# Optimization experiments

Measured on AMD Instinct MI355X. Metric: run time of the kernel, lower is better.

## Reference

```python
import jax, jax.numpy as jnp
from jax import lax
import numpy as np

BLANK = 0
PAD = 1
LABEL_SMOOTHING = 0.1
CE_SCALE = 1.0
TEMPERATURE = 1.0

B, T, U1, D, V = 8, 128, 33, 512, 4096  # U1 = U + 1


def setup_inputs() -> dict:
    key = jax.random.key(0)
    k0, k1, k2, k3, k4 = jax.random.split(key, 5)
    x = jax.random.normal(k0, (B, T, U1, D), dtype=jnp.float32)
    weight = jax.random.normal(k1, (V, D), dtype=jnp.float32) * 0.02
    bias = jnp.zeros((V,), dtype=jnp.float32)
    src_lengths = jax.random.randint(k2, (B,), T // 2, T + 1, dtype=jnp.int32)
    tgt_lengths = jax.random.randint(k3, (B,), U1 // 2, U1, dtype=jnp.int32)
    targets = jax.random.randint(k4, (B, U1 - 1), 2, V, dtype=jnp.int32)
    pos = jnp.arange(U1 - 1, dtype=jnp.int32)
    targets = jnp.where(pos[None, :] < tgt_lengths[:, None], targets, PAD)
    return {'x': x, 'weight': weight, 'bias': bias, 'targets': targets,
            'src_lengths': src_lengths, 'tgt_lengths': tgt_lengths}


def _rnnt_neglogp(blank_lp, emit_lp, src_lengths, tgt_lengths):
    """RNN-T forward DP. blank_lp: (B,T,U1) log P(blank); emit_lp: (B,T,U) log P(y_u).
    Returns per-utterance negative log-likelihood, shape (B,)."""
    Bn, Tn, U1n = blank_lp.shape
    # alpha at t=0: can only emit labels -> prefix-sum of emit log-probs
    alpha0 = jnp.concatenate(
        [jnp.zeros((Bn, 1), blank_lp.dtype), jnp.cumsum(emit_lp[:, 0, :], axis=1)], axis=1)

    def t_step(alpha_prev, xs):
        blank_prev, emit_t = xs  # (B,U1), (B,U)
        a = alpha_prev + blank_prev  # blank transition from t-1
        def u_step(c, xu):
            a_u, e_prev = xu  # each (B,)
            c = jnp.logaddexp(a_u, c + e_prev)  # emit transition from u-1 at same t
            return c, c
        _, rest = lax.scan(u_step, a[:, 0], (a[:, 1:].T, emit_t.T))  # rest: (U,B)
        alpha_t = jnp.concatenate([a[:, :1], rest.T], axis=1)
        return alpha_t, alpha_t

    xs = (jnp.swapaxes(blank_lp[:, :-1], 0, 1), jnp.swapaxes(emit_lp[:, 1:], 0, 1))
    _, alphas_rest = lax.scan(t_step, alpha0, xs)  # (T-1,B,U1)
    alphas = jnp.concatenate([alpha0[None], alphas_rest], axis=0)  # (T,B,U1)
    bidx = jnp.arange(Bn)
    alpha_last_t = alphas[src_lengths - 1, bidx]  # (B,U1)
    a_fin = jnp.take_along_axis(alpha_last_t, tgt_lengths[:, None], axis=1)[:, 0]
    b_fin = blank_lp[bidx, src_lengths - 1, tgt_lengths]  # final blank emission
    return -(a_fin + b_fin)


def reference(x, weight, bias, targets, src_lengths, tgt_lengths):
    Vn = weight.shape[0]
    # joint logits over full lattice: (B,T,U1,V)
    logits = (jnp.einsum('btud,vd->btuv', x, weight) + bias).astype(jnp.float32)
    lp = jax.nn.log_softmax(logits / TEMPERATURE, axis=-1)
    blank_lp = lp[..., BLANK]  # (B,T,U1)
    emit_lp = jnp.take_along_axis(lp[:, :, :-1, :], targets[:, None, :, None].astype(jnp.int32), axis=3)[..., 0]  # (B,T,U)
    loss_prob = jnp.sum(_rnnt_neglogp(blank_lp, emit_lp, src_lengths, tgt_lengths))
    loss_delay = jnp.zeros((), jnp.float32)  # delay_func == 'zero'
    # label-smoothed CE on last valid encoder frame
    last_h = jnp.take_along_axis(x, (src_lengths - 1)[:, None, None, None], axis=1)[:, 0]  # (B,U1,D)
    last_h = last_h[:, :-1]  # (B,U,D)
    ce_logits = (jnp.einsum('bud,vd->buv', last_h, weight) + bias).astype(jnp.float32)
    lprobs = jax.nn.log_softmax(ce_logits, axis=-1)
    nll = -jnp.take_along_axis(lprobs, targets[..., None], axis=-1)[..., 0]  # (B,U)
    smooth = -jnp.sum(lprobs, axis=-1)
    mask = (targets != PAD).astype(lprobs.dtype)
    eps_i = LABEL_SMOOTHING / (Vn - 1)
    loss_smoothed = jnp.sum(((1.0 - LABEL_SMOOTHING - eps_i) * nll + eps_i * smooth) * mask)
    total = loss_prob + loss_delay + CE_SCALE * loss_smoothed
    return total
```

## Files before the change

### kernel.cpp

```cpp
#include <hip/hip_runtime.h>
#include <hip/hip_bf16.h>
#include <math.h>
#include <stdint.h>

#define B_ 8
#define T_ 128
#define U1_ 33
#define D_ 512
#define V_ 4096
#define M_ (B_*T_*U1_)

#define BLANK_ 0
#define PAD_ 1

#define TM 128
#define TN 128
#define BKB 128
#define NK (D_/BKB)
#define GN (V_/TN)

typedef __attribute__((ext_vector_type(4))) float fvec4;
typedef __attribute__((ext_vector_type(8))) int   i8v;
typedef __attribute__((ext_vector_type(4))) int   i4v;

#define SCALE_A 0x7F7F7F7Fu
#define SCALE_B 0x79797979u

__device__ __forceinline__ void load_lds16(const uint8_t* g, uint8_t* l) {
    __builtin_amdgcn_global_load_lds(
        (const __attribute__((address_space(1))) unsigned int*)g,
        (__attribute__((address_space(3))) unsigned int*)l, 16, 0, 0);
}

__device__ __forceinline__ unsigned pack4_fp8(fvec4 v) {
    int r = __builtin_amdgcn_cvt_pk_fp8_f32(v.x, v.y, 0, false);
    r = __builtin_amdgcn_cvt_pk_fp8_f32(v.z, v.w, r, true);
    return (unsigned)r;
}

__global__ void convert_kernel(const float* __restrict__ x, const float* __restrict__ w,
                               uint8_t* __restrict__ xf8, uint8_t* __restrict__ wf8)
{
    int i = blockIdx.x * 256 + threadIdx.x;
    int stride = gridDim.x * 256;
    const int nx = (M_ * D_) / 16;
    const int nw = (V_ * D_) / 16;
    for (int j = i; j < nx; j += stride) {
        const fvec4* p = (const fvec4*)x + (size_t)j * 4;
        uint4 o = { pack4_fp8(p[0]), pack4_fp8(p[1]), pack4_fp8(p[2]), pack4_fp8(p[3]) };
        ((uint4*)xf8)[j] = o;
    }
    for (int j = i; j < nw; j += stride) {
        const fvec4* p = (const fvec4*)w + (size_t)j * 4;
        fvec4 v0 = p[0]*64.0f, v1 = p[1]*64.0f, v2 = p[2]*64.0f, v3 = p[3]*64.0f;
        uint4 o = { pack4_fp8(v0), pack4_fp8(v1), pack4_fp8(v2), pack4_fp8(v3) };
        ((uint4*)wf8)[j] = o;
    }
}

__global__ __launch_bounds__(256, 2)
void gemm_fused(const uint8_t* __restrict__ xf8, const uint8_t* __restrict__ wf8,
                const float* __restrict__ bias, const int* __restrict__ targets,
                float* __restrict__ partial_e, float* __restrict__ partial_z,
                float* __restrict__ blank_z, float* __restrict__ emit_z)
{
    __shared__ __align__(16) uint8_t As[2][TM * BKB];
    __shared__ __align__(16) uint8_t Bs[2][TN * BKB];
    __shared__ float ps[TM], pz[TM];
    __shared__ int tgt_s[TM];

    const int tid  = threadIdx.x;
    const int lane = tid & 63;
    const int wid  = tid >> 6;
    const int m0   = blockIdx.x * TM;
    const int n0   = blockIdx.y * TN;

    const int srow = wid * 32 + (lane >> 3);
    const int schk = (lane & 7) ^ ((lane >> 3) & 7);
    const uint8_t* agp = xf8 + (size_t)(m0 + srow) * D_ + schk * 16;
    const uint8_t* bgp = wf8 + (size_t)(n0 + srow) * D_ + schk * 16;

    fvec4 acc[4][4];
#pragma unroll
    for (int i = 0; i < 4; i++)
#pragma unroll
        for (int j = 0; j < 4; j++) acc[i][j] = (fvec4)0.0f;

    const int wrow = (wid >> 1) * 64;
    const int wcol = (wid & 1) * 64;
    const int m15  = lane & 15;
    const int quad = lane >> 4;

    auto stage = [&](int buf, int ks) {
        const uint8_t* ag = agp + ks * BKB;
        const uint8_t* bg = bgp + ks * BKB;
#pragma unroll
        for (int j = 0; j < 4; j++) {
            load_lds16(ag + j * 8 * D_, &As[buf][(wid * 32 + j * 8) * BKB]);
            load_lds16(bg + j * 8 * D_, &Bs[buf][(wid * 32 + j * 8) * BKB]);
        }
    };

    stage(0, 0);
    __syncthreads();

    const int e   = m15 & 7;
    const int c0b = (((quad << 1) ^ e) << 4);

    for (int ks = 0; ks < NK; ks++) {
        const int cur = ks & 1;
        if (ks + 1 < NK) stage(cur ^ 1, ks + 1);

        i8v fa[4], fb[4];
#pragma unroll
        for (int mi = 0; mi < 4; mi++) {
            int base = (wrow + mi * 16 + m15) << 7;
            union { i4v h[2]; i8v w; } u;
            u.h[0] = *(const i4v*)&As[cur][base + c0b];
            u.h[1] = *(const i4v*)&As[cur][base + (c0b ^ 16)];
            fa[mi] = u.w;
        }
#pragma unroll
        for (int ni = 0; ni < 4; ni++) {
            int base = (wcol + ni * 16 + m15) << 7;
            union { i4v h[2]; i8v w; } u;
            u.h[0] = *(const i4v*)&Bs[cur][base + c0b];
            u.h[1] = *(const i4v*)&Bs[cur][base + (c0b ^ 16)];
            fb[ni] = u.w;
        }
#pragma unroll
        for (int mi = 0; mi < 4; mi++)
#pragma unroll
            for (int ni = 0; ni < 4; ni++)
                acc[mi][ni] = __builtin_amdgcn_mfma_scale_f32_16x16x128_f8f6f4(
                                  fa[mi], fb[ni], acc[mi][ni],
                                  0, 0,
                                  0, SCALE_A, 0, SCALE_B);
        __syncthreads();
    }

    if (tid < TM) {
        ps[tid] = 0.0f; pz[tid] = 0.0f;
        int row = m0 + tid;
        int u = row % U1_;
        int b = row / (T_ * U1_);
        tgt_s[tid] = (u < U1_ - 1) ? targets[b * (U1_ - 1) + u] : -1;
    }
    __syncthreads();

    float bv[4];
#pragma unroll
    for (int ni = 0; ni < 4; ni++) bv[ni] = bias[n0 + wcol + ni * 16 + m15];

    const bool blank_lane = (blockIdx.y == 0) && (wcol == 0) && (m15 == 0);

#pragma unroll
    for (int mi = 0; mi < 4; mi++) {
#pragma unroll
        for (int r = 0; r < 4; r++) {
            const int irow = wrow + mi * 16 + quad * 4 + r;
            float se = 0.0f, sz = 0.0f;
#pragma unroll
            for (int ni = 0; ni < 4; ni++) {
                float z = acc[mi][ni][r] + bv[ni];
                se += __expf(z);
                sz += z;
                int c = n0 + wcol + ni * 16 + m15;
                if (tgt_s[irow] == c) emit_z[m0 + irow] = z;
            }
            if (blank_lane) blank_z[m0 + irow] = acc[mi][0][r] + bv[0];
            se += __shfl_xor(se, 1, 64); sz += __shfl_xor(sz, 1, 64);
            se += __shfl_xor(se, 2, 64); sz += __shfl_xor(sz, 2, 64);
            se += __shfl_xor(se, 4, 64); sz += __shfl_xor(sz, 4, 64);
            se += __shfl_xor(se, 8, 64); sz += __shfl_xor(sz, 8, 64);
            if (m15 == 0) { atomicAdd(&ps[irow], se); atomicAdd(&pz[irow], sz); }
        }
    }
    __syncthreads();
    if (tid < TM) {
        partial_e[(size_t)blockIdx.y * M_ + m0 + tid] = ps[tid];
        partial_z[(size_t)blockIdx.y * M_ + m0 + tid] = pz[tid];
    }
}

__global__ void lse_combine(const float* __restrict__ partial_e, const float* __restrict__ partial_z,
                            const float* __restrict__ emit_z, const int* __restrict__ targets,
                            const int* __restrict__ src_lengths,
                            float* __restrict__ lse, float* __restrict__ out)
{
    int r = blockIdx.x * 256 + threadIdx.x;
    float se = 0.0f, sz = 0.0f;
#pragma unroll
    for (int j = 0; j < GN; j++) {
        se += partial_e[(size_t)j * M_ + r];
        sz += partial_z[(size_t)j * M_ + r];
    }
    float l = __logf(se);
    lse[r] = l;

    int b   = r / (T_ * U1_);
    int rem = r % (T_ * U1_);
    int t   = rem / U1_;
    int u   = rem % U1_;
    if (u < U1_ - 1 && t == src_lengths[b] - 1) {
        int tgt = targets[b * (U1_ - 1) + u];
        if (tgt != PAD_) {
            float nll    = l - emit_z[r];
            float smooth = (float)V_ * l - sz;
            const float eps_i = 0.1f / (float)(V_ - 1);
            atomicAdd(out, (1.0f - 0.1f - eps_i) * nll + eps_i * smooth);
        }
    }
}

__global__ __launch_bounds__(256)
void dp_kernel(const float* __restrict__ blank_z, const float* __restrict__ emit_z,
               const float* __restrict__ lse, const int* __restrict__ src_lengths,
               const int* __restrict__ tgt_lengths, float* __restrict__ out)
{
    __shared__ float blp[T_ * U1_];
    __shared__ float elp[T_ * U1_];
    const int tid = threadIdx.x;
    const int b = blockIdx.x;
    for (int i = tid; i < T_ * U1_; i += 256) {
        int g = b * T_ * U1_ + i;
        float l = lse[g];
        blp[i] = blank_z[g] - l;
        elp[i] = emit_z[g] - l;
    }
    __syncthreads();
    if (tid >= 64) return;

    const int u = tid;
    const int ua = (u < U1_) ? u : U1_ - 1;
    const int sl = src_lengths[b], tl = tgt_lengths[b];

    float val = 0.0f;
    float afin = 0.0f;

    for (int d = 1; d <= (T_ - 1) + (U1_ - 1); d++) {
        int t = d - u;
        int tb = t - 1; tb = tb < 0 ? 0 : (tb > T_ - 1 ? T_ - 1 : tb);
        int tc = t < 0 ? 0 : (t > T_ - 1 ? T_ - 1 : t);
        float blv = blp[tb * U1_ + ua];
        float elv = elp[tc * U1_ + (ua > 0 ? ua - 1 : 0)];
        float up = __shfl_up(val, 1, 64);
        bool valid = (u < U1_) && (t >= 0) && (t < T_);
        if (valid) {
            if (t == 0) {
                val = up + elv;
            } else if (u == 0) {
                val = val + blv;
            } else {
                float a1 = val + blv;
                float a2 = up + elv;
                float mx = fmaxf(a1, a2), mn = fminf(a1, a2);
                val = mx + log1pf(__expf(mn - mx));
            }
            if (t == sl - 1 && u == tl) afin = val;
        }
    }
#pragma unroll
    for (int off = 1; off < 64; off <<= 1) afin += __shfl_xor(afin, off, 64);
    if (u == 0) {
        float bfin = blp[(sl - 1) * U1_ + tl];
        atomicAdd(out, -(afin + bfin));
    }
}

extern "C" void kernel_launch(void* const* d_in, const int* in_sizes, int n_in,
                              void* d_out, int out_size, void* d_ws, size_t ws_size,
                              hipStream_t stream)
{
    const float* x           = (const float*)d_in[0];
    const float* w           = (const float*)d_in[1];
    const float* bias        = (const float*)d_in[2];
    const int*   targets     = (const int*)d_in[3];
    const int*   src_lengths = (const int*)d_in[4];
    const int*   tgt_lengths = (const int*)d_in[5];
    float* out = (float*)d_out;

    char* p = (char*)d_ws;
    uint8_t* xf8 = (uint8_t*)p;     p += (size_t)M_ * D_;
    uint8_t* wf8 = (uint8_t*)p;     p += (size_t)V_ * D_;
    float* partial_e = (float*)p;   p += (size_t)GN * M_ * sizeof(float);
    float* partial_z = (float*)p;   p += (size_t)GN * M_ * sizeof(float);
    float* lse       = (float*)p;   p += (size_t)M_ * sizeof(float);
    float* blank_z   = (float*)p;   p += (size_t)M_ * sizeof(float);
    float* emit_z    = (float*)p;   p += (size_t)M_ * sizeof(float);

    hipMemsetAsync(out, 0, sizeof(float), stream);

    convert_kernel<<<1536, 256, 0, stream>>>(x, w, xf8, wf8);
    gemm_fused<<<dim3(M_/TM, V_/TN), 256, 0, stream>>>(xf8, wf8, bias, targets,
                                                       partial_e, partial_z, blank_z, emit_z);
    lse_combine<<<M_/256, 256, 0, stream>>>(partial_e, partial_z, emit_z, targets,
                                            src_lengths, lse, out);
    dp_kernel<<<B_, 256, 0, stream>>>(blank_z, emit_z, lse, src_lengths, tgt_lengths, out);
}
```

Baseline: 364.7 us.

## Keep A tile resident in LDS and loop over N tiles per block

After: 600.5 us. 1.65x slower.

```diff
diff --git a/kernel.cpp b/kernel.cpp
--- a/kernel.cpp
+++ b/kernel.cpp
@@ -14,10 +14,11 @@
 #define PAD_ 1
 
 #define TM 128
-#define TN 128
+#define TNS 256
 #define BKB 128
-#define NK (D_/BKB)
-#define GN (V_/TN)
+#define NKS (D_/BKB)
+#define GY 4
+#define NTILES (V_/(GY*TNS))
 
 typedef __attribute__((ext_vector_type(4))) float fvec4;
 typedef __attribute__((ext_vector_type(8))) int   i8v;
@@ -58,14 +59,14 @@
     }
 }
 
-__global__ __launch_bounds__(256, 2)
+__global__ __launch_bounds__(512, 2)
 void gemm_fused(const uint8_t* __restrict__ xf8, const uint8_t* __restrict__ wf8,
                 const float* __restrict__ bias, const int* __restrict__ targets,
                 float* __restrict__ partial_e, float* __restrict__ partial_z,
                 float* __restrict__ blank_z, float* __restrict__ emit_z)
 {
-    __shared__ __align__(16) uint8_t As[2][TM * BKB];
-    __shared__ __align__(16) uint8_t Bs[2][TN * BKB];
+    __shared__ __align__(16) uint8_t As[NKS][TM * BKB];
+    __shared__ __align__(16) uint8_t Bs[2][TNS * BKB];
     __shared__ float ps[TM], pz[TM];
     __shared__ int tgt_s[TM];
 
@@ -73,71 +74,25 @@
     const int lane = tid & 63;
     const int wid  = tid >> 6;
     const int m0   = blockIdx.x * TM;
-    const int n0   = blockIdx.y * TN;
-
-    const int srow = wid * 32 + (lane >> 3);
+    const int nslice = blockIdx.y;
+
     const int schk = (lane & 7) ^ ((lane >> 3) & 7);
-    const uint8_t* agp = xf8 + (size_t)(m0 + srow) * D_ + schk * 16;
-    const uint8_t* bgp = wf8 + (size_t)(n0 + srow) * D_ + schk * 16;
-
-    fvec4 acc[4][4];
-#pragma unroll
-    for (int i = 0; i < 4; i++)
-#pragma unroll
-        for (int j = 0; j < 4; j++) acc[i][j] = (fvec4)0.0f;
-
-    const int wrow = (wid >> 1) * 64;
-    const int wcol = (wid & 1) * 64;
-    const int m15  = lane & 15;
-    const int quad = lane >> 4;
-
-    auto stage = [&](int buf, int ks) {
-        const uint8_t* ag = agp + ks * BKB;
-        const uint8_t* bg = bgp + ks * BKB;
-#pragma unroll
-        for (int j = 0; j < 4; j++) {
-            load_lds16(ag + j * 8 * D_, &As[buf][(wid * 32 + j * 8) * BKB]);
+
+    auto stageB = [&](int buf, int nt, int ks) {
+        const uint8_t* bg = wf8 + (size_t)(nslice * (GY==4?1024:V_/GY) + nt * TNS
+                                           + wid * 32 + (lane >> 3)) * D_
+                                + ks * BKB + schk * 16;
+#pragma unroll
+        for (int j = 0; j < 4; j++)
             load_lds16(bg + j * 8 * D_, &Bs[buf][(wid * 32 + j * 8) * BKB]);
-        }
     };
-
-    stage(0, 0);
-    __syncthreads();
-
-    const int e   = m15 & 7;
-    const int c0b = (((quad << 1) ^ e) << 4);
-
-    for (int ks = 0; ks < NK; ks++) {
-        const int cur = ks & 1;
-        if (ks + 1 < NK) stage(cur ^ 1, ks + 1);
-
-        i8v fa[4], fb[4];
-#pragma unroll
-        for (int mi = 0; mi < 4; mi++) {
-            int base = (wrow + mi * 16 + m15) << 7;
-            union { i4v h[2]; i8v w; } u;
-            u.h[0] = *(const i4v*)&As[cur][base + c0b];
-            u.h[1] = *(const i4v*)&As[cur][base + (c0b ^ 16)];
-            fa[mi] = u.w;
-        }
-#pragma unroll
-        for (int ni = 0; ni < 4; ni++) {
-            int base = (wcol + ni * 16 + m15) << 7;
-            union { i4v h[2]; i8v w; } u;
-            u.h[0] = *(const i4v*)&Bs[cur][base + c0b];
-            u.h[1] = *(const i4v*)&Bs[cur][base + (c0b ^ 16)];
-            fb[ni] = u.w;
-        }
-#pragma unroll
-        for (int mi = 0; mi < 4; mi++)
-#pragma unroll
-            for (int ni = 0; ni < 4; ni++)
-                acc[mi][ni] = __builtin_amdgcn_mfma_scale_f32_16x16x128_f8f6f4(
-                                  fa[mi], fb[ni], acc[mi][ni],
-                                  0, 0,
-                                  0, SCALE_A, 0, SCALE_B);
-        __syncthreads();
-    }
+    auto stageA = [&](int ks) {
+        const uint8_t* ag = xf8 + (size_t)(m0 + wid * 16 + (lane >> 3)) * D_
+                                + ks * BKB + schk * 16;
+#pragma unroll
+        for (int j = 0; j < 2; j++)
+            load_lds16(ag + j * 8 * D_, &As[ks][(wid * 16 + j * 8) * BKB]);
+    };
 
     if (tid < TM) {
         ps[tid] = 0.0f; pz[tid] = 0.0f;
@@ -146,40 +101,95 @@
         int b = row / (T_ * U1_);
         tgt_s[tid] = (u < U1_ - 1) ? targets[b * (U1_ - 1) + u] : -1;
     }
+#pragma unroll
+    for (int ks = 0; ks < NKS; ks++) stageA(ks);
+    stageB(0, 0, 0);
     __syncthreads();
 
-    float bv[4];
-#pragma unroll
-    for (int ni = 0; ni < 4; ni++) bv[ni] = bias[n0 + wcol + ni * 16 + m15];
-
-    const bool blank_lane = (blockIdx.y == 0) && (wcol == 0) && (m15 == 0);
-
-#pragma unroll
-    for (int mi = 0; mi < 4; mi++) {
-#pragma unroll
-        for (int r = 0; r < 4; r++) {
-            const int irow = wrow + mi * 16 + quad * 4 + r;
-            float se = 0.0f, sz = 0.0f;
+    const int wrow = (wid >> 2) * 64;
+    const int wcol = (wid & 3) * 64;
+    const int m15  = lane & 15;
+    const int quad = lane >> 4;
+    const int e    = m15 & 7;
+    const int c0b  = (((quad << 1) ^ e) << 4);
+
+    int cur = 0;
+    for (int nt = 0; nt < NTILES; nt++) {
+        fvec4 acc[4][4];
+#pragma unroll
+        for (int i = 0; i < 4; i++)
+#pragma unroll
+            for (int j = 0; j < 4; j++) acc[i][j] = (fvec4)0.0f;
+
+#pragma unroll
+        for (int ks = 0; ks < NKS; ks++) {
+            if (ks < NKS - 1)           stageB(cur ^ 1, nt, ks + 1);
+            else if (nt < NTILES - 1)   stageB(cur ^ 1, nt + 1, 0);
+
+            i8v fa[4], fb[4];
+#pragma unroll
+            for (int mi = 0; mi < 4; mi++) {
+                int base = (wrow + mi * 16 + m15) << 7;
+                union { i4v h[2]; i8v w; } u;
+                u.h[0] = *(const i4v*)&As[ks][base + c0b];
+                u.h[1] = *(const i4v*)&As[ks][base + (c0b ^ 16)];
+                fa[mi] = u.w;
+            }
 #pragma unroll
             for (int ni = 0; ni < 4; ni++) {
-                float z = acc[mi][ni][r] + bv[ni];
-                se += __expf(z);
-                sz += z;
-                int c = n0 + wcol + ni * 16 + m15;
-                if (tgt_s[irow] == c) emit_z[m0 + irow] = z;
+                int base = (wcol + ni * 16 + m15) << 7;
+                union { i4v h[2]; i8v w; } u;
+                u.h[0] = *(const i4v*)&Bs[cur][base + c0b];
+                u.h[1] = *(const i4v*)&Bs[cur][base + (c0b ^ 16)];
+                fb[ni] = u.w;
             }
-            if (blank_lane) blank_z[m0 + irow] = acc[mi][0][r] + bv[0];
-            se += __shfl_xor(se, 1, 64); sz += __shfl_xor(sz, 1, 64);
-            se += __shfl_xor(se, 2, 64); sz += __shfl_xor(sz, 2, 64);
-            se += __shfl_xor(se, 4, 64); sz += __shfl_xor(sz, 4, 64);
-            se += __shfl_xor(se, 8, 64); sz += __shfl_xor(sz, 8, 64);
-            if (m15 == 0) { atomicAdd(&ps[irow], se); atomicAdd(&pz[irow], sz); }
+#pragma unroll
+            for (int mi = 0; mi < 4; mi++)
+#pragma unroll
+                for (int ni = 0; ni < 4; ni++)
+                    acc[mi][ni] = __builtin_amdgcn_mfma_scale_f32_16x16x128_f8f6f4(
+                                      fa[mi], fb[ni], acc[mi][ni],
+                                      0, 0,
+                                      0, SCALE_A, 0, SCALE_B);
+            __syncthreads();
+            cur ^= 1;
         }
-    }
+
+        const int nbase = nslice * (V_ / GY) + nt * TNS;
+        float bv[4];
+#pragma unroll
+        for (int ni = 0; ni < 4; ni++) bv[ni] = bias[nbase + wcol + ni * 16 + m15];
+
+        const bool blank_lane = (nslice == 0) && (nt == 0) && (wcol == 0) && (m15 == 0);
+
+#pragma unroll
+        for (int mi = 0; mi < 4; mi++) {
+#pragma unroll
+            for (int r = 0; r < 4; r++) {
+                const int irow = wrow + mi * 16 + quad * 4 + r;
+                float se = 0.0f, sz = 0.0f;
+#pragma unroll
+                for (int ni = 0; ni < 4; ni++) {
+                    float z = acc[mi][ni][r] + bv[ni];
+                    se += __expf(z);
+                    sz += z;
+                    int c = nbase + wcol + ni * 16 + m15;
+                    if (tgt_s[irow] == c) emit_z[m0 + irow] = z;
+                }
+                if (blank_lane) blank_z[m0 + irow] = acc[mi][0][r] + bv[0];
+                se += __shfl_xor(se, 1, 64); sz += __shfl_xor(sz, 1, 64);
+                se += __shfl_xor(se, 2, 64); sz += __shfl_xor(sz, 2, 64);
+                se += __shfl_xor(se, 4, 64); sz += __shfl_xor(sz, 4, 64);
+                se += __shfl_xor(se, 8, 64); sz += __shfl_xor(sz, 8, 64);
+                if (m15 == 0) { atomicAdd(&ps[irow], se); atomicAdd(&pz[irow], sz); }
+            }
+        }
+    }
+
     __syncthreads();
     if (tid < TM) {
-        partial_e[(size_t)blockIdx.y * M_ + m0 + tid] = ps[tid];
-        partial_z[(size_t)blockIdx.y * M_ + m0 + tid] = pz[tid];
+        partial_e[(size_t)nslice * M_ + m0 + tid] = ps[tid];
+        partial_z[(size_t)nslice * M_ + m0 + tid] = pz[tid];
     }
 }
 
@@ -191,7 +201,7 @@
     int r = blockIdx.x * 256 + threadIdx.x;
     float se = 0.0f, sz = 0.0f;
 #pragma unroll
-    for (int j = 0; j < GN; j++) {
+    for (int j = 0; j < GY; j++) {
         se += partial_e[(size_t)j * M_ + r];
         sz += partial_z[(size_t)j * M_ + r];
     }
@@ -283,8 +293,8 @@
     char* p = (char*)d_ws;
     uint8_t* xf8 = (uint8_t*)p;     p += (size_t)M_ * D_;
     uint8_t* wf8 = (uint8_t*)p;     p += (size_t)V_ * D_;
-    float* partial_e = (float*)p;   p += (size_t)GN * M_ * sizeof(float);
-    float* partial_z = (float*)p;   p += (size_t)GN * M_ * sizeof(float);
+    float* partial_e = (float*)p;   p += (size_t)GY * M_ * sizeof(float);
+    float* partial_z = (float*)p;   p += (size_t)GY * M_ * sizeof(float);
     float* lse       = (float*)p;   p += (size_t)M_ * sizeof(float);
     float* blank_z   = (float*)p;   p += (size_t)M_ * sizeof(float);
     float* emit_z    = (float*)p;   p += (size_t)M_ * sizeof(float);
@@ -292,8 +302,8 @@
     hipMemsetAsync(out, 0, sizeof(float), stream);
 
     convert_kernel<<<1536, 256, 0, stream>>>(x, w, xf8, wf8);
-    gemm_fused<<<dim3(M_/TM, V_/TN), 256, 0, stream>>>(xf8, wf8, bias, targets,
-                                                       partial_e, partial_z, blank_z, emit_z);
+    gemm_fused<<<dim3(M_/TM, GY), 512, 0, stream>>>(xf8, wf8, bias, targets,
+                                                    partial_e, partial_z, blank_z, emit_z);
     lse_combine<<<M_/256, 256, 0, stream>>>(partial_e, partial_z, emit_z, targets,
                                             src_lengths, lse, out);
     dp_kernel<<<B_, 256, 0, stream>>>(blank_z, emit_z, lse, src_lengths, tgt_lengths, out);
```

## Compute smoothing logit sum via column-summed weights and tighten GEMM pipeline barriers

Applied to the files above, without the earlier changes.

Result: slower. 452.4 us (+24.0%).

```diff
diff --git a/kernel.cpp b/kernel.cpp
--- a/kernel.cpp
+++ b/kernel.cpp
@@ -58,15 +58,34 @@
     }
 }
 
+__global__ void wsum_kernel(const float* __restrict__ w, const float* __restrict__ bias,
+                            float* __restrict__ wsum)
+{
+    const int t = threadIdx.x;
+    const int v0 = blockIdx.x * 128;
+    float s0 = 0.0f, s1 = 0.0f;
+    for (int v = 0; v < 128; v++) {
+        s0 += w[(size_t)(v0 + v) * D_ + t];
+        s1 += w[(size_t)(v0 + v) * D_ + t + 256];
+    }
+    atomicAdd(&wsum[t], s0);
+    atomicAdd(&wsum[t + 256], s1);
+    if (blockIdx.x == 0) {
+        float b = 0.0f;
+        for (int v = t; v < V_; v += 256) b += bias[v];
+        atomicAdd(&wsum[D_], b);
+    }
+}
+
 __global__ __launch_bounds__(256, 2)
 void gemm_fused(const uint8_t* __restrict__ xf8, const uint8_t* __restrict__ wf8,
                 const float* __restrict__ bias, const int* __restrict__ targets,
-                float* __restrict__ partial_e, float* __restrict__ partial_z,
+                float* __restrict__ partial_e,
                 float* __restrict__ blank_z, float* __restrict__ emit_z)
 {
     __shared__ __align__(16) uint8_t As[2][TM * BKB];
     __shared__ __align__(16) uint8_t Bs[2][TN * BKB];
-    __shared__ float ps[TM], pz[TM];
+    __shared__ float ps[TM];
     __shared__ int tgt_s[TM];
 
     const int tid  = threadIdx.x;
@@ -102,6 +121,13 @@
     };
 
     stage(0, 0);
+    if (tid < TM) {
+        ps[tid] = 0.0f;
+        int row = m0 + tid;
+        int u = row % U1_;
+        int b = row / (T_ * U1_);
+        tgt_s[tid] = (u < U1_ - 1) ? targets[b * (U1_ - 1) + u] : -1;
+    }
     __syncthreads();
 
     const int e   = m15 & 7;
@@ -109,7 +135,14 @@
 
     for (int ks = 0; ks < NK; ks++) {
         const int cur = ks & 1;
-        if (ks + 1 < NK) stage(cur ^ 1, ks + 1);
+        if (ks + 1 < NK) {
+            stage(cur ^ 1, ks + 1);
+            asm volatile("s_waitcnt vmcnt(8)" ::: "memory");
+        } else {
+            asm volatile("s_waitcnt vmcnt(0)" ::: "memory");
+        }
+        __builtin_amdgcn_sched_barrier(0);
+        __builtin_amdgcn_s_barrier();
 
         i8v fa[4], fb[4];
 #pragma unroll
@@ -136,17 +169,9 @@
                                   fa[mi], fb[ni], acc[mi][ni],
                                   0, 0,
                                   0, SCALE_A, 0, SCALE_B);
-        __syncthreads();
-    }
-
-    if (tid < TM) {
-        ps[tid] = 0.0f; pz[tid] = 0.0f;
-        int row = m0 + tid;
-        int u = row % U1_;
-        int b = row / (T_ * U1_);
-        tgt_s[tid] = (u < U1_ - 1) ? targets[b * (U1_ - 1) + u] : -1;
-    }
-    __syncthreads();
+        __builtin_amdgcn_s_barrier();
+        __builtin_amdgcn_sched_barrier(0);
+    }
 
     float bv[4];
 #pragma unroll
@@ -159,42 +184,38 @@
 #pragma unroll
         for (int r = 0; r < 4; r++) {
             const int irow = wrow + mi * 16 + quad * 4 + r;
-            float se = 0.0f, sz = 0.0f;
+            float se = 0.0f;
 #pragma unroll
             for (int ni = 0; ni < 4; ni++) {
                 float z = acc[mi][ni][r] + bv[ni];
                 se += __expf(z);
-                sz += z;
                 int c = n0 + wcol + ni * 16 + m15;
                 if (tgt_s[irow] == c) emit_z[m0 + irow] = z;
             }
             if (blank_lane) blank_z[m0 + irow] = acc[mi][0][r] + bv[0];
-            se += __shfl_xor(se, 1, 64); sz += __shfl_xor(sz, 1, 64);
-            se += __shfl_xor(se, 2, 64); sz += __shfl_xor(sz, 2, 64);
-            se += __shfl_xor(se, 4, 64); sz += __shfl_xor(sz, 4, 64);
-            se += __shfl_xor(se, 8, 64); sz += __shfl_xor(sz, 8, 64);
-            if (m15 == 0) { atomicAdd(&ps[irow], se); atomicAdd(&pz[irow], sz); }
+            se += __shfl_xor(se, 1, 64);
+            se += __shfl_xor(se, 2, 64);
+            se += __shfl_xor(se, 4, 64);
+            se += __shfl_xor(se, 8, 64);
+            if (m15 == 0) atomicAdd(&ps[irow], se);
         }
     }
     __syncthreads();
     if (tid < TM) {
         partial_e[(size_t)blockIdx.y * M_ + m0 + tid] = ps[tid];
-        partial_z[(size_t)blockIdx.y * M_ + m0 + tid] = pz[tid];
-    }
-}
-
-__global__ void lse_combine(const float* __restrict__ partial_e, const float* __restrict__ partial_z,
+    }
+}
+
+__global__ void lse_combine(const float* __restrict__ partial_e,
                             const float* __restrict__ emit_z, const int* __restrict__ targets,
                             const int* __restrict__ src_lengths,
+                            const float* __restrict__ x, const float* __restrict__ wsum,
                             float* __restrict__ lse, float* __restrict__ out)
 {
     int r = blockIdx.x * 256 + threadIdx.x;
-    float se = 0.0f, sz = 0.0f;
-#pragma unroll
-    for (int j = 0; j < GN; j++) {
-        se += partial_e[(size_t)j * M_ + r];
-        sz += partial_z[(size_t)j * M_ + r];
-    }
+    float se = 0.0f;
+#pragma unroll
+    for (int j = 0; j < GN; j++) se += partial_e[(size_t)j * M_ + r];
     float l = __logf(se);
     lse[r] = l;
 
@@ -205,6 +226,14 @@
     if (u < U1_ - 1 && t == src_lengths[b] - 1) {
         int tgt = targets[b * (U1_ - 1) + u];
         if (tgt != PAD_) {
+            float sz = wsum[D_];
+            const fvec4* xr = (const fvec4*)(x + (size_t)r * D_);
+            const fvec4* ws = (const fvec4*)wsum;
+#pragma unroll 4
+            for (int d = 0; d < D_ / 4; d++) {
+                fvec4 a = xr[d], wv = ws[d];
+                sz += a.x * wv.x + a.y * wv.y + a.z * wv.z + a.w * wv.w;
+            }
             float nll    = l - emit_z[r];
             float smooth = (float)V_ * l - sz;
             const float eps_i = 0.1f / (float)(V_ - 1);
@@ -284,17 +313,19 @@
     uint8_t* xf8 = (uint8_t*)p;     p += (size_t)M_ * D_;
     uint8_t* wf8 = (uint8_t*)p;     p += (size_t)V_ * D_;
     float* partial_e = (float*)p;   p += (size_t)GN * M_ * sizeof(float);
-    float* partial_z = (float*)p;   p += (size_t)GN * M_ * sizeof(float);
     float* lse       = (float*)p;   p += (size_t)M_ * sizeof(float);
     float* blank_z   = (float*)p;   p += (size_t)M_ * sizeof(float);
     float* emit_z    = (float*)p;   p += (size_t)M_ * sizeof(float);
+    float* wsum      = (float*)p;   p += (size_t)(D_ + 4) * sizeof(float);
 
     hipMemsetAsync(out, 0, sizeof(float), stream);
+    hipMemsetAsync(wsum, 0, (D_ + 4) * sizeof(float), stream);
 
     convert_kernel<<<1536, 256, 0, stream>>>(x, w, xf8, wf8);
+    wsum_kernel<<<32, 256, 0, stream>>>(w, bias, wsum);
     gemm_fused<<<dim3(M_/TM, V_/TN), 256, 0, stream>>>(xf8, wf8, bias, targets,
-                                                       partial_e, partial_z, blank_z, emit_z);
-    lse_combine<<<M_/256, 256, 0, stream>>>(partial_e, partial_z, emit_z, targets,
-                                            src_lengths, lse, out);
+                                                       partial_e, blank_z, emit_z);
+    lse_combine<<<M_/256, 256, 0, stream>>>(partial_e, emit_z, targets,
+                                            src_lengths, x, wsum, lse, out);
     dp_kernel<<<B_, 256, 0, stream>>>(blank_z, emit_z, lse, src_lengths, tgt_lengths, out);
 }
```
